# Performance work log

Measured on AMD Instinct MI355X. Metric: run time of the kernel, lower is better.

## Reference

```python
import jax, jax.numpy as jnp
import numpy as np

B, L, D = 1, 2048, 2048
H, KVH, HD = 16, 4, 128
E, TOPK, G, TKG = 16, 4, 4, 2   # experts, top_k, n_group, topk_group
I, SH_I = 1024, 2048            # moe_intermediate, shared intermediate (1024*2)
EPS = 1e-5
THETA = 1e6
SCALE = HD ** -0.5
RSF = 2.5                        # routed_scaling_factor


def rms(x, w):
    return x * jax.lax.rsqrt(jnp.mean(x * x, axis=-1, keepdims=True) + EPS) * w


def rope(x):
    # x: [B, n_heads, L, HD], non-traditional (split-half) RoPE
    pos = jnp.arange(x.shape[2], dtype=jnp.float32)
    inv = 1.0 / (THETA ** (jnp.arange(0, HD, 2, dtype=jnp.float32) / HD))
    ang = pos[:, None] * inv[None, :]                    # [L, HD/2]
    cos, sin = jnp.cos(ang), jnp.sin(ang)
    x1, x2 = x[..., : HD // 2], x[..., HD // 2 :]
    return jnp.concatenate([x1 * cos - x2 * sin, x2 * cos + x1 * sin], axis=-1)


def setup_inputs() -> dict:
    key = jax.random.key(0)
    ks = jax.random.split(key, 13)
    s = 0.02
    mk = lambda k, shp: jax.random.normal(k, shp, jnp.float32) * s
    return {
        'x': jax.random.normal(ks[0], (B, L, D), jnp.float32),
        'w_q': mk(ks[1], (H * HD, D)),
        'w_k': mk(ks[2], (KVH * HD, D)),
        'w_v': mk(ks[3], (KVH * HD, D)),
        'w_o': mk(ks[4], (D, H * HD)),
        'q_norm_w': jnp.ones(HD, jnp.float32),
        'k_norm_w': jnp.ones(HD, jnp.float32),
        'ln1_w': jnp.ones(D, jnp.float32),
        'ln2_w': jnp.ones(D, jnp.float32),
        'gate_w': mk(ks[5], (E, D)),
        'gate_bias': mk(ks[6], (E,)),
        'wg': mk(ks[7], (E, I, D)),
        'wu': mk(ks[8], (E, I, D)),
        'wd': mk(ks[9], (E, D, I)),
        'sh_g': mk(ks[10], (SH_I, D)),
        'sh_u': mk(ks[11], (SH_I, D)),
        'sh_d': mk(ks[12], (D, SH_I)),
    }


def reference(x, w_q, w_k, w_v, w_o, q_norm_w, k_norm_w, ln1_w, ln2_w,
              gate_w, gate_bias, wg, wu, wd, sh_g, sh_u, sh_d):
    # ---- attention block ----
    h = rms(x, ln1_w)
    q = rms((h @ w_q.T).reshape(B, L, H, HD), q_norm_w).transpose(0, 2, 1, 3)
    k = rms((h @ w_k.T).reshape(B, L, KVH, HD), k_norm_w).transpose(0, 2, 1, 3)
    v = (h @ w_v.T).reshape(B, L, KVH, HD).transpose(0, 2, 1, 3)
    q, k = rope(q), rope(k)
    rep = H // KVH
    k = jnp.repeat(k, rep, axis=1)
    v = jnp.repeat(v, rep, axis=1)
    causal = jnp.tril(jnp.ones((L, L), bool))
    logits = jnp.einsum('bhqd,bhkd->bhqk', q, k) * SCALE
    logits = jnp.where(causal, logits, jnp.float32(-1e30))
    attn = jax.nn.softmax(logits, axis=-1)
    o = jnp.einsum('bhqk,bhkd->bhqd', attn, v).transpose(0, 2, 1, 3).reshape(B, L, H * HD)
    h1 = x + o @ w_o.T

    # ---- MoE block ----
    t = rms(h1, ln2_w).reshape(B * L, D)
    T = t.shape[0]
    # group-limited top-k gate (noaux_tc)
    sc = jax.nn.sigmoid(t @ gate_w.T)                    # [T, E] original scores
    s2 = sc + gate_bias
    sg = s2.reshape(T, G, E // G)
    group_scores = jax.lax.top_k(sg, 2)[0].sum(-1)       # [T, G]
    gidx = jax.lax.top_k(group_scores, TKG)[1]           # keep TKG best groups
    gmask = jnp.zeros((T, G), jnp.float32).at[jnp.arange(T)[:, None], gidx].set(1.0)
    masked = (sg * gmask[..., None]).reshape(T, E)       # dropped groups -> 0
    inds = jax.lax.top_k(masked, TOPK)[1]                # [T, TOPK]
    w = jnp.take_along_axis(sc, inds, axis=-1)
    w = w / (w.sum(-1, keepdims=True) + 1e-20) * RSF
    # combine weights scattered into [T, E]
    C = jnp.zeros((T, E), jnp.float32).at[jnp.arange(T)[:, None], inds].add(w)
    # expert SwiGLU (dense over experts, masked combine -> identical math)
    g = jnp.einsum('td,eid->tei', t, wg)
    u = jnp.einsum('td,eid->tei', t, wu)
    hm = jax.nn.silu(g) * u                               # [T, E, I]
    y = jnp.einsum('tei,edi,te->td', hm, wd, C)
    # shared experts
    sh = (jax.nn.silu(t @ sh_g.T) * (t @ sh_u.T)) @ sh_d.T
    return h1 + (y + sh).reshape(B, L, D)
```

## Files before the change

### kernel.cpp

```cpp
#include <hip/hip_runtime.h>
#include <math.h>

#define TT 2048
#define DM 2048
#define NHD 16
#define NKV 4
#define HDIM 128
#define NI 1024
#define ATT_SCALE 0.08838834764831845f

typedef unsigned short u16;
typedef __attribute__((ext_vector_type(8))) short short8;
typedef __attribute__((ext_vector_type(4))) short short4v;
typedef __attribute__((ext_vector_type(4))) float float4v;

#define AS1 __attribute__((address_space(1)))
#define AS3 __attribute__((address_space(3)))

__device__ __forceinline__ u16 f2bf(float f) {
  union { float f; unsigned u; } v; v.f = f;
  unsigned r = v.u + 0x7fffu + ((v.u >> 16) & 1u);
  return (u16)(r >> 16);
}
__device__ __forceinline__ float bf2f(u16 h) {
  union { unsigned u; float f; } v; v.u = ((unsigned)h) << 16;
  return v.f;
}
__device__ __forceinline__ float4v mfma16(short8 a, short8 b, float4v c) {
  return __builtin_amdgcn_mfma_f32_16x16x32_bf16(a, b, c, 0, 0, 0);
}
__device__ __forceinline__ void gl_lds(const u16* g, u16* l) {
  __builtin_amdgcn_global_load_lds((const AS1 void*)g, (AS3 void*)l, 16, 0, 0);
}

__global__ void cvt_split(const float* __restrict__ s, u16* __restrict__ oh,
                          u16* __restrict__ ol, int n) {
  int i = (blockIdx.x * 256 + threadIdx.x) * 4;
  if (i >= n) return;
  float4v v = *(const float4v*)(s + i);
  short4v vh, vl;
  #pragma unroll
  for (int c = 0; c < 4; ++c) {
    u16 hb = f2bf(v[c]);
    vh[c] = (short)hb;
    vl[c] = (short)f2bf(v[c] - bf2f(hb));
  }
  *(short4v*)(oh + i) = vh;
  *(short4v*)(ol + i) = vl;
}

__global__ void cvt_plain(const float* __restrict__ s, u16* __restrict__ o, int n) {
  int i = (blockIdx.x * 256 + threadIdx.x) * 8;
  if (i >= n) return;
  float4v v0 = *(const float4v*)(s + i);
  float4v v1 = *(const float4v*)(s + i + 4);
  short8 ov;
  #pragma unroll
  for (int c = 0; c < 4; ++c) {
    ov[c] = (short)f2bf(v0[c]);
    ov[c + 4] = (short)f2bf(v1[c]);
  }
  *(short8*)(o + i) = ov;
}

__global__ void rms_kernel(const float* __restrict__ in, const float* __restrict__ w,
                           u16* oh, u16* ol, float* of, u16* ob) {
  const int row = blockIdx.x, tid = threadIdx.x;
  const int lane = tid & 63, wvi = tid >> 6;
  const float* xr = in + (long)row * DM;
  float4v a = *(const float4v*)(xr + tid * 4);
  float4v b = *(const float4v*)(xr + 1024 + tid * 4);
  float ss = a[0]*a[0] + a[1]*a[1] + a[2]*a[2] + a[3]*a[3]
           + b[0]*b[0] + b[1]*b[1] + b[2]*b[2] + b[3]*b[3];
  #pragma unroll
  for (int m = 1; m < 64; m <<= 1) ss += __shfl_xor(ss, m);
  __shared__ float red[4];
  if (lane == 0) red[wvi] = ss;
  __syncthreads();
  float tot = red[0] + red[1] + red[2] + red[3];
  float sc = 1.0f / sqrtf(tot * (1.0f / 2048.0f) + 1e-5f);
  float4v w0 = *(const float4v*)(w + tid * 4);
  float4v w1 = *(const float4v*)(w + 1024 + tid * 4);
  #pragma unroll
  for (int c = 0; c < 4; ++c) {
    float v0 = a[c] * sc * w0[c];
    float v1 = b[c] * sc * w1[c];
    long i0 = (long)row * DM + tid * 4 + c;
    long i1 = i0 + 1024;
    if (oh) {
      u16 h0 = f2bf(v0); oh[i0] = h0; ol[i0] = f2bf(v0 - bf2f(h0));
      u16 h1 = f2bf(v1); oh[i1] = h1; ol[i1] = f2bf(v1 - bf2f(h1));
    }
    if (of) { of[i0] = v0; of[i1] = v1; }
    if (ob) { ob[i0] = f2bf(v0); ob[i1] = f2bf(v1); }
  }
}

__global__ void rope_kernel(const float* __restrict__ qlin, const float* __restrict__ klin,
                            const float* __restrict__ qw, const float* __restrict__ kw,
                            u16* qh, u16* ql, u16* kh, u16* kl) {
  int rw = blockIdx.x * 4 + (threadIdx.x >> 6);
  int lane = threadIdx.x & 63;
  int t = rw / 20, hh = rw - t * 20;
  const float* src; const float* nw; u16 *dh, *dl;
  if (hh < 16) {
    long ofs = (long)t * 2048 + hh * 128;
    src = qlin + ofs; nw = qw; dh = qh + ofs; dl = ql + ofs;
  } else {
    long ofs = (long)t * 512 + (hh - 16) * 128;
    src = klin + ofs; nw = kw; dh = kh + ofs; dl = kl + ofs;
  }
  float x1 = src[lane], x2 = src[lane + 64];
  float ss = x1 * x1 + x2 * x2;
  #pragma unroll
  for (int m = 1; m < 64; m <<= 1) ss += __shfl_xor(ss, m);
  float sc = 1.0f / sqrtf(ss * (1.0f / 128.0f) + 1e-5f);
  x1 *= sc * nw[lane];
  x2 *= sc * nw[lane + 64];
  double inv = pow(1.0e6, -(double)lane * (1.0 / 64.0));
  double ang = (double)t * inv;
  float cs = (float)cos(ang), sn = (float)sin(ang);
  float o1 = x1 * cs - x2 * sn;
  float o2 = x2 * cs + x1 * sn;
  u16 hb1 = f2bf(o1); dh[lane] = hb1;      dl[lane] = f2bf(o1 - bf2f(hb1));
  u16 hb2 = f2bf(o2); dh[lane + 64] = hb2; dl[lane + 64] = f2bf(o2 - bf2f(hb2));
}

struct GemmP {
  const u16* Ah; long aloOff;
  const u16* B0h; const u16* B1h; long blo0; long blo1; long bstride; int ns0;
  int K;
  const int* permA; const int* cnt; const int* offs;
  int fixedM; int maxRow;
  float* oF; int ldF;
  float* oF2; int ldF2; int osplit;
  u16* oB; long oBlo; int ldB;
  const float* addX;
  const u16* dslots; const int* inv;
};

template<int EPI, bool SPLIT>
__launch_bounds__(256, 2)
__global__ void gemm_bt(GemmP p) {
  const int e = blockIdx.z;
  const int cnt = p.cnt ? p.cnt[e] : p.fixedM;
  const int mt0 = blockIdx.x * 128;
  if (mt0 >= cnt) return;
  const int off = p.offs ? p.offs[e] : 0;
  const int nt0 = blockIdx.y * 128;

  __shared__ u16 lAh[128 * 64];
  __shared__ u16 lBh[128 * 64];
  __shared__ u16 lAl[SPLIT ? 128 * 64 : 8];
  __shared__ u16 lBl[SPLIT ? 128 * 64 : 8];

  const int tid = threadIdx.x;
  const int lane = tid & 63, wvi = tid >> 6;
  const int quad = lane >> 4, l16 = lane & 15;
  const int wm = (wvi >> 1) * 64, wn = (wvi & 1) * 64;
  const int srow = tid >> 3;
  const int scc = (tid & 7) ^ (srow & 7);

  const u16* agp[4];
  #pragma unroll
  for (int i = 0; i < 4; ++i) {
    int m = mt0 + i * 32 + srow;
    int r = off + m; if (r > p.maxRow) r = p.maxRow;
    if (p.permA) r = p.permA[r];
    agp[i] = p.Ah + (long)r * p.K + scc * 8;
  }
  const u16* bgph[4]; const u16* bgpl[4];
  #pragma unroll
  for (int j = 0; j < 4; ++j) {
    int n = nt0 + j * 32 + srow;
    const u16* bp; long lo;
    if (n < p.ns0) { bp = p.B0h + (long)e * p.bstride + (long)n * p.K; lo = p.blo0; }
    else           { bp = p.B1h + (long)e * p.bstride + (long)(n - p.ns0) * p.K; lo = p.blo1; }
    bgph[j] = bp + scc * 8;
    bgpl[j] = bp + lo + scc * 8;
  }

  float4v acc[4][4];
  #pragma unroll
  for (int a = 0; a < 4; ++a)
    #pragma unroll
    for (int b = 0; b < 4; ++b)
      acc[a][b] = (float4v){0.f, 0.f, 0.f, 0.f};

  const int wofs = wvi * 64 * 8;

  for (int k0 = 0; k0 < p.K; k0 += 64) {
    __syncthreads();
    #pragma unroll
    for (int i = 0; i < 4; ++i) {
      gl_lds(agp[i] + k0, &lAh[i * 2048 + wofs]);
      if constexpr (SPLIT) gl_lds(agp[i] + p.aloOff + k0, &lAl[i * 2048 + wofs]);
    }
    #pragma unroll
    for (int j = 0; j < 4; ++j) {
      gl_lds(bgph[j] + k0, &lBh[j * 2048 + wofs]);
      if constexpr (SPLIT) gl_lds(bgpl[j] + k0, &lBl[j * 2048 + wofs]);
    }
    __syncthreads();
    #pragma unroll
    for (int kc = 0; kc < 2; ++kc) {
      short8 ah[4], al[4], bh[4], bl[4];
      #pragma unroll
      for (int t = 0; t < 4; ++t) {
        int m = wm + t * 16 + l16;
        int ia = (m * 8 + ((kc * 4 + quad) ^ (m & 7))) * 8;
        ah[t] = *(const short8*)&lAh[ia];
        if constexpr (SPLIT) al[t] = *(const short8*)&lAl[ia];
        int n = wn + t * 16 + l16;
        int ib = (n * 8 + ((kc * 4 + quad) ^ (n & 7))) * 8;
        bh[t] = *(const short8*)&lBh[ib];
        if constexpr (SPLIT) bl[t] = *(const short8*)&lBl[ib];
      }
      #pragma unroll
      for (int mt = 0; mt < 4; ++mt)
        #pragma unroll
        for (int nt = 0; nt < 4; ++nt) {
          acc[mt][nt] = mfma16(ah[mt], bh[nt], acc[mt][nt]);
          if constexpr (SPLIT) {
            acc[mt][nt] = mfma16(ah[mt], bl[nt], acc[mt][nt]);
            acc[mt][nt] = mfma16(al[mt], bh[nt], acc[mt][nt]);
          }
        }
    }
  }

  #pragma unroll
  for (int mt = 0; mt < 4; ++mt) {
    #pragma unroll
    for (int nt = 0; nt < 4; ++nt) {
      const int n = nt0 + wn + nt * 16 + l16;
      const int mlb = wm + mt * 16 + quad * 4;
      if constexpr (EPI == 1) {
        short4v vh, vl;
        #pragma unroll
        for (int r = 0; r < 4; ++r) {
          float v = acc[mt][nt][r];
          u16 hb = f2bf(v);
          vh[r] = (short)hb;
          vl[r] = (short)f2bf(v - bf2f(hb));
        }
        long ix = (long)n * p.ldB + (mt0 + mlb);
        *(short4v*)&p.oB[ix] = vh;
        *(short4v*)&p.oB[ix + p.oBlo] = vl;
      } else {
        #pragma unroll
        for (int r = 0; r < 4; ++r) {
          const int gm = mt0 + mlb + r;
          if (gm >= cnt) continue;
          float v = acc[mt][nt][r];
          if constexpr (EPI == 0) {
            if (n < p.osplit) p.oF[(long)gm * p.ldF + n] = v;
            else p.oF2[(long)gm * p.ldF2 + (n - p.osplit)] = v;
          } else if constexpr (EPI == 2) {
            long ix = (long)gm * p.ldF + n;
            p.oF[ix] = v + p.addX[ix];
          } else if constexpr (EPI == 3) {
            p.oB[(long)(off + gm) * p.ldB + n] = f2bf(v);
          } else if constexpr (EPI == 5) {
            long ix = (long)gm * p.ldF + n;
            const int* iv = p.inv + gm * 4;
            float s = bf2f(p.dslots[(long)iv[0] * DM + n])
                    + bf2f(p.dslots[(long)iv[1] * DM + n])
                    + bf2f(p.dslots[(long)iv[2] * DM + n])
                    + bf2f(p.dslots[(long)iv[3] * DM + n]);
            p.oF[ix] = v + p.addX[ix] + s;
          }
        }
      }
    }
  }
}

__launch_bounds__(256, 2)
__global__ void attn_kernel(const u16* __restrict__ qh, const u16* __restrict__ ql,
                            const u16* __restrict__ kh, const u16* __restrict__ kl,
                            const u16* __restrict__ vh, const u16* __restrict__ vl,
                            u16* __restrict__ oh, u16* __restrict__ ol) {
  const int head = blockIdx.x;
  const int qt = 31 - (int)blockIdx.y;
  const int kvh = head >> 2;
  const int tid = threadIdx.x;
  const int lane = tid & 63, wvi = tid >> 6;
  const int quad = lane >> 4, l16 = lane & 15;

  __shared__ u16 lKh[64 * 128];
  __shared__ u16 lKl[64 * 128];
  __shared__ u16 lVh[128 * 64];
  __shared__ u16 lVl[128 * 64];
  __shared__ u16 lP[4][2][16 * 64];
  u16* Ph = &lP[wvi][0][0];
  u16* Pl = &lP[wvi][1][0];

  const int qbase = qt * 64;
  const int qrow0 = qbase + wvi * 16;
  short8 qfh[4], qfl[4];
  {
    int row = qrow0 + l16;
    const u16* ph = qh + (long)row * (NHD * HDIM) + head * HDIM + quad * 8;
    const u16* pl = ql + (long)row * (NHD * HDIM) + head * HDIM + quad * 8;
    #pragma unroll
    for (int kc = 0; kc < 4; ++kc) {
      qfh[kc] = *(const short8*)(ph + kc * 32);
      qfl[kc] = *(const short8*)(pl + kc * 32);
    }
  }
  float4v oacc[8];
  #pragma unroll
  for (int dt = 0; dt < 8; ++dt) oacc[dt] = (float4v){0.f, 0.f, 0.f, 0.f};
  float mrun[4], lrun[4];
  #pragma unroll
  for (int r = 0; r < 4; ++r) { mrun[r] = -INFINITY; lrun[r] = 0.f; }

  const int sck = (tid & 15) ^ (tid >> 4);
  const int scv = (tid & 7) ^ ((tid >> 3) & 7);
  const int nsteps = qt + 1;

  for (int kt = 0; kt < nsteps; ++kt) {
    const int t0 = kt * 64;
    __syncthreads();
    #pragma unroll
    for (int i = 0; i < 4; ++i) {
      int krow = i * 16 + (tid >> 4);
      long kg = (long)(t0 + krow) * (NKV * HDIM) + kvh * HDIM + sck * 8;
      gl_lds(kh + kg, &lKh[(i * 256 + wvi * 64) * 8]);
      gl_lds(kl + kg, &lKl[(i * 256 + wvi * 64) * 8]);
      int vrow = i * 32 + (tid >> 3);
      long vg = (long)(kvh * HDIM + vrow) * TT + t0 + scv * 8;
      gl_lds(vh + vg, &lVh[(i * 256 + wvi * 64) * 8]);
      gl_lds(vl + vg, &lVl[(i * 256 + wvi * 64) * 8]);
    }
    __syncthreads();

    float4v s[4];
    #pragma unroll
    for (int nt = 0; nt < 4; ++nt) s[nt] = (float4v){0.f, 0.f, 0.f, 0.f};
    #pragma unroll
    for (int kc = 0; kc < 4; ++kc) {
      #pragma unroll
      for (int nt = 0; nt < 4; ++nt) {
        int n = nt * 16 + l16;
        int idx = (n * 16 + ((kc * 4 + quad) ^ (n & 15))) * 8;
        short8 bh = *(const short8*)&lKh[idx];
        short8 bl = *(const short8*)&lKl[idx];
        s[nt] = mfma16(qfh[kc], bh, s[nt]);
        s[nt] = mfma16(qfh[kc], bl, s[nt]);
        s[nt] = mfma16(qfl[kc], bh, s[nt]);
      }
    }

    const bool dg = (kt == qt);
    #pragma unroll
    for (int nt = 0; nt < 4; ++nt)
      #pragma unroll
      for (int r = 0; r < 4; ++r) {
        float v = s[nt][r] * ATT_SCALE;
        if (dg) {
          int kcol = t0 + nt * 16 + l16;
          int qrow = qrow0 + quad * 4 + r;
          if (kcol > qrow) v = -1e30f;
        }
        s[nt][r] = v;
      }

    float alf[4];
    #pragma unroll
    for (int r = 0; r < 4; ++r) {
      float mx = fmaxf(fmaxf(s[0][r], s[1][r]), fmaxf(s[2][r], s[3][r]));
      mx = fmaxf(mx, __shfl_xor(mx, 1));
      mx = fmaxf(mx, __shfl_xor(mx, 2));
      mx = fmaxf(mx, __shfl_xor(mx, 4));
      mx = fmaxf(mx, __shfl_xor(mx, 8));
      float mnew = fmaxf(mrun[r], mx);
      float al = expf(mrun[r] - mnew);
      float ps = 0.f;
      #pragma unroll
      for (int nt = 0; nt < 4; ++nt) {
        float pv = expf(s[nt][r] - mnew);
        s[nt][r] = pv;
        ps += pv;
      }
      ps += __shfl_xor(ps, 1); ps += __shfl_xor(ps, 2);
      ps += __shfl_xor(ps, 4); ps += __shfl_xor(ps, 8);
      lrun[r] = lrun[r] * al + ps;
      mrun[r] = mnew;
      alf[r] = al;
    }
    #pragma unroll
    for (int dt = 0; dt < 8; ++dt)
      #pragma unroll
      for (int r = 0; r < 4; ++r)
        oacc[dt][r] *= alf[r];

    #pragma unroll
    for (int nt = 0; nt < 4; ++nt)
      #pragma unroll
      for (int r = 0; r < 4; ++r) {
        int row = quad * 4 + r;
        int col = nt * 16 + l16;
        int idx = (row * 8 + ((col >> 3) ^ (row & 7))) * 8 + (col & 7);
        float pv = s[nt][r];
        u16 hb = f2bf(pv);
        Ph[idx] = hb;
        Pl[idx] = f2bf(pv - bf2f(hb));
      }

    #pragma unroll
    for (int kc = 0; kc < 2; ++kc) {
      int idxp = (l16 * 8 + ((kc * 4 + quad) ^ (l16 & 7))) * 8;
      short8 ph = *(const short8*)&Ph[idxp];
      short8 pl = *(const short8*)&Pl[idxp];
      #pragma unroll
      for (int dt = 0; dt < 8; ++dt) {
        int d = dt * 16 + l16;
        int idx = (d * 8 + ((kc * 4 + quad) ^ (d & 7))) * 8;
        short8 wh = *(const short8*)&lVh[idx];
        short8 wl = *(const short8*)&lVl[idx];
        oacc[dt] = mfma16(ph, wh, oacc[dt]);
        oacc[dt] = mfma16(ph, wl, oacc[dt]);
        oacc[dt] = mfma16(pl, wh, oacc[dt]);
      }
    }
  }

  #pragma unroll
  for (int dt = 0; dt < 8; ++dt)
    #pragma unroll
    for (int r = 0; r < 4; ++r) {
      int row = qrow0 + quad * 4 + r;
      int d = dt * 16 + l16;
      float v = oacc[dt][r] / lrun[r];
      long ix = (long)row * (NHD * HDIM) + head * HDIM + d;
      u16 hb = f2bf(v);
      oh[ix] = hb;
      ol[ix] = f2bf(v - bf2f(hb));
    }
}

__global__ void routing_kernel(const float* __restrict__ t32, const float* __restrict__ gw,
                               const float* __restrict__ gb,
                               int* inds, float* wv, int* counts) {
  int t = blockIdx.x;
  int lane = threadIdx.x;
  const float* tr = t32 + (long)t * DM;
  float4v tv[8];
  #pragma unroll
  for (int j = 0; j < 8; ++j) tv[j] = *(const float4v*)(tr + lane * 32 + j * 4);
  float sc[16];
  for (int e = 0; e < 16; ++e) {
    const float* g = gw + (long)e * DM + lane * 32;
    float acc = 0.f;
    #pragma unroll
    for (int j = 0; j < 8; ++j) {
      float4v gv = *(const float4v*)(g + j * 4);
      acc += tv[j][0]*gv[0] + tv[j][1]*gv[1] + tv[j][2]*gv[2] + tv[j][3]*gv[3];
    }
    #pragma unroll
    for (int m = 1; m < 64; m <<= 1) acc += __shfl_xor(acc, m);
    sc[e] = 1.f / (1.f + expf(-acc));
  }
  if (lane == 0) {
    float s2[16];
    for (int e = 0; e < 16; ++e) s2[e] = sc[e] + gb[e];
    float gs[4];
    for (int g = 0; g < 4; ++g) {
      float xq[4] = { s2[4*g], s2[4*g+1], s2[4*g+2], s2[4*g+3] };
      int am = 0; float m1 = xq[0];
      for (int i = 1; i < 4; ++i) if (xq[i] > m1) { m1 = xq[i]; am = i; }
      float m2 = -1e30f;
      for (int i = 0; i < 4; ++i) if (i != am) m2 = fmaxf(m2, xq[i]);
      gs[g] = m1 + m2;
    }
    int g0 = 0;
    for (int g = 1; g < 4; ++g) if (gs[g] > gs[g0]) g0 = g;
    int g1 = -1;
    for (int g = 0; g < 4; ++g) if (g != g0 && (g1 < 0 || gs[g] > gs[g1])) g1 = g;
    float msk[16];
    for (int e = 0; e < 16; ++e) {
      int g = e >> 2;
      msk[e] = (g == g0 || g == g1) ? s2[e] : 0.0f;
    }
    int id[4]; float w[4]; float wsum = 0.f;
    for (int j = 0; j < 4; ++j) {
      int bi = 0; float bv = msk[0];
      for (int e = 1; e < 16; ++e) if (msk[e] > bv) { bv = msk[e]; bi = e; }
      id[j] = bi; w[j] = sc[bi]; msk[bi] = -1e30f;
      wsum += w[j];
    }
    float scale = 2.5f / (wsum + 1e-20f);
    for (int j = 0; j < 4; ++j) {
      inds[t * 4 + j] = id[j];
      wv[t * 4 + j] = w[j] * scale;
      atomicAdd(&counts[id[j]], 1);
    }
  }
}

__global__ void scan_kernel(int* ctrl) {
  if (threadIdx.x == 0) {
    int a = 0;
    for (int e = 0; e < 16; ++e) { ctrl[16 + e] = a; a += ctrl[e]; }
  }
}

__global__ void assign_kernel(const int* inds, const float* wv, int* ctrl,
                              int* perm, float* wslot, int* inv) {
  int t = blockIdx.x * 256 + threadIdx.x;
  if (t >= TT) return;
  for (int j = 0; j < 4; ++j) {
    int e = inds[t * 4 + j];
    int pos = atomicAdd(&ctrl[32 + e], 1);
    int s = ctrl[16 + e] + pos;
    perm[s] = t;
    wslot[s] = wv[t * 4 + j];
    inv[t * 4 + j] = s;
  }
}

__global__ void hm_moe_kernel(const u16* __restrict__ gu, const float* __restrict__ wslot,
                              u16* __restrict__ hm) {
  int slot = blockIdx.x;
  int i = threadIdx.x * 4;
  float w = wslot[slot];
  const u16* gp = gu + (long)slot * 2048;
  short4v gv = *(const short4v*)(gp + i);
  short4v uv = *(const short4v*)(gp + 1024 + i);
  short4v ov;
  #pragma unroll
  for (int c = 0; c < 4; ++c) {
    float g = bf2f((u16)gv[c]);
    float u = bf2f((u16)uv[c]);
    float h = g / (1.f + expf(-g)) * u * w;
    ov[c] = (short)f2bf(h);
  }
  *(short4v*)&hm[(long)slot * 1024 + i] = ov;
}

__global__ void hm_sh_kernel(const u16* __restrict__ gu, u16* __restrict__ hm) {
  int t = blockIdx.x;
  int i = threadIdx.x * 8;
  const u16* gp = gu + (long)t * 4096 + i;
  const u16* up = gu + (long)t * 4096 + 2048 + i;
  u16* op = hm + (long)t * 2048 + i;
  #pragma unroll
  for (int c = 0; c < 2; ++c) {
    short4v gv = *(const short4v*)(gp + c * 4);
    short4v uv = *(const short4v*)(up + c * 4);
    short4v ov;
    #pragma unroll
    for (int q = 0; q < 4; ++q) {
      float g = bf2f((u16)gv[q]);
      float u = bf2f((u16)uv[q]);
      float h = g / (1.f + expf(-g)) * u;
      ov[q] = (short)f2bf(h);
    }
    *(short4v*)(op + c * 4) = ov;
  }
}

extern "C" void kernel_launch(void* const* d_in, const int* in_sizes, int n_in,
                              void* d_out, int out_size, void* d_ws, size_t ws_size,
                              hipStream_t stream) {
  (void)in_sizes; (void)n_in; (void)out_size; (void)ws_size;
  const float* x   = (const float*)d_in[0];
  const float* wq  = (const float*)d_in[1];
  const float* wk  = (const float*)d_in[2];
  const float* wvv = (const float*)d_in[3];
  const float* wo  = (const float*)d_in[4];
  const float* qnw = (const float*)d_in[5];
  const float* knw = (const float*)d_in[6];
  const float* ln1 = (const float*)d_in[7];
  const float* ln2 = (const float*)d_in[8];
  const float* gw  = (const float*)d_in[9];
  const float* gb  = (const float*)d_in[10];
  const float* wg  = (const float*)d_in[11];
  const float* wu  = (const float*)d_in[12];
  const float* wd  = (const float*)d_in[13];
  const float* shg = (const float*)d_in[14];
  const float* shu = (const float*)d_in[15];
  const float* shd = (const float*)d_in[16];
  float* out = (float*)d_out;

  char* wp = (char*)d_ws;
  auto alloc = [&](size_t b) -> char* { char* r = wp; wp += (b + 255) & ~(size_t)255; return r; };
  u16* h_hi   = (u16*)alloc((size_t)TT * DM * 2);
  u16* h_lo   = (u16*)alloc((size_t)TT * DM * 2);
  float* q_lin = (float*)alloc((size_t)TT * 2048 * 4);
  float* k_lin = (float*)alloc((size_t)TT * 512 * 4);
  u16* q_hi   = (u16*)alloc((size_t)TT * 2048 * 2);
  u16* q_lo   = (u16*)alloc((size_t)TT * 2048 * 2);
  u16* k_hi   = (u16*)alloc((size_t)TT * 512 * 2);
  u16* k_lo   = (u16*)alloc((size_t)TT * 512 * 2);
  u16* vT_hi  = (u16*)alloc((size_t)512 * TT * 2);
  u16* vT_lo  = (u16*)alloc((size_t)512 * TT * 2);
  u16* o_hi   = (u16*)alloc((size_t)TT * 2048 * 2);
  u16* o_lo   = (u16*)alloc((size_t)TT * 2048 * 2);
  float* h1   = (float*)alloc((size_t)TT * DM * 4);
  float* t32  = (float*)alloc((size_t)TT * DM * 4);
  u16* t_bf   = (u16*)alloc((size_t)TT * DM * 2);
  u16* gu_sh  = (u16*)alloc((size_t)TT * 4096 * 2);
  u16* hm_sh  = (u16*)alloc((size_t)TT * 2048 * 2);
  u16* gu_moe = (u16*)alloc((size_t)8192 * 2048 * 2);
  u16* hm_moe = (u16*)alloc((size_t)8192 * 1024 * 2);
  u16* dtmp   = (u16*)alloc((size_t)8192 * 2048 * 2);
  int* inds   = (int*)alloc((size_t)TT * 4 * 4);
  float* wvals = (float*)alloc((size_t)TT * 4 * 4);
  int* ctrl   = (int*)alloc(256);
  int* perm   = (int*)alloc(8192 * 4);
  float* wslot = (float*)alloc(8192 * 4);
  int* inv    = (int*)alloc((size_t)TT * 4 * 4);
  const int NQ = 2048 * 2048, NK = 512 * 2048;
  u16* wq_c  = (u16*)alloc((size_t)NQ * 2 * 2);
  u16* wk_c  = (u16*)alloc((size_t)NK * 2 * 2);
  u16* wv_c  = (u16*)alloc((size_t)NK * 2 * 2);
  u16* wo_c  = (u16*)alloc((size_t)NQ * 2 * 2);
  const int NGU = 16 * NI * DM;
  u16* wg_c  = (u16*)alloc((size_t)NGU * 2);
  u16* wu_c  = (u16*)alloc((size_t)NGU * 2);
  u16* wd_c  = (u16*)alloc((size_t)NGU * 2);
  u16* shg_c = (u16*)alloc((size_t)NQ * 2);
  u16* shu_c = (u16*)alloc((size_t)NQ * 2);
  u16* shd_c = (u16*)alloc((size_t)NQ * 2);

  hipMemsetAsync(ctrl, 0, 256, stream);

  cvt_split<<<NQ / 4 / 256, 256, 0, stream>>>(wq, wq_c, wq_c + NQ, NQ);
  cvt_split<<<NK / 4 / 256, 256, 0, stream>>>(wk, wk_c, wk_c + NK, NK);
  cvt_split<<<NK / 4 / 256, 256, 0, stream>>>(wvv, wv_c, wv_c + NK, NK);
  cvt_split<<<NQ / 4 / 256, 256, 0, stream>>>(wo, wo_c, wo_c + NQ, NQ);
  cvt_plain<<<NGU / 8 / 256, 256, 0, stream>>>(wg, wg_c, NGU);
  cvt_plain<<<NGU / 8 / 256, 256, 0, stream>>>(wu, wu_c, NGU);
  cvt_plain<<<NGU / 8 / 256, 256, 0, stream>>>(wd, wd_c, NGU);
  cvt_plain<<<NQ / 8 / 256, 256, 0, stream>>>(shg, shg_c, NQ);
  cvt_plain<<<NQ / 8 / 256, 256, 0, stream>>>(shu, shu_c, NQ);
  cvt_plain<<<NQ / 8 / 256, 256, 0, stream>>>(shd, shd_c, NQ);

  rms_kernel<<<TT, 256, 0, stream>>>(x, ln1, h_hi, h_lo, nullptr, nullptr);

  { GemmP p{}; p.Ah = h_hi; p.aloOff = h_lo - h_hi;
    p.B0h = wq_c; p.blo0 = NQ; p.B1h = wk_c; p.blo1 = NK; p.ns0 = 2048;
    p.K = DM; p.fixedM = TT; p.maxRow = TT - 1;
    p.oF = q_lin; p.ldF = 2048; p.oF2 = k_lin; p.ldF2 = 512; p.osplit = 2048;
    gemm_bt<0, true><<<dim3(16, 20, 1), 256, 0, stream>>>(p); }

  { GemmP p{}; p.Ah = h_hi; p.aloOff = h_lo - h_hi;
    p.B0h = wv_c; p.blo0 = NK; p.B1h = wv_c; p.blo1 = NK; p.ns0 = 1 << 30;
    p.K = DM; p.fixedM = TT; p.maxRow = TT - 1;
    p.oB = vT_hi; p.oBlo = vT_lo - vT_hi; p.ldB = TT;
    gemm_bt<1, true><<<dim3(16, 4, 1), 256, 0, stream>>>(p); }

  rope_kernel<<<TT * 20 / 4, 256, 0, stream>>>(q_lin, k_lin, qnw, knw, q_hi, q_lo, k_hi, k_lo);

  attn_kernel<<<dim3(NHD, 32, 1), 256, 0, stream>>>(q_hi, q_lo, k_hi, k_lo, vT_hi, vT_lo, o_hi, o_lo);

  { GemmP p{}; p.Ah = o_hi; p.aloOff = o_lo - o_hi;
    p.B0h = wo_c; p.blo0 = NQ; p.B1h = wo_c; p.blo1 = NQ; p.ns0 = 1 << 30;
    p.K = DM; p.fixedM = TT; p.maxRow = TT - 1;
    p.oF = h1; p.ldF = 2048; p.addX = x;
    gemm_bt<2, true><<<dim3(16, 16, 1), 256, 0, stream>>>(p); }

  rms_kernel<<<TT, 256, 0, stream>>>(h1, ln2, nullptr, nullptr, t32, t_bf);

  routing_kernel<<<TT, 64, 0, stream>>>(t32, gw, gb, inds, wvals, ctrl);
  scan_kernel<<<1, 64, 0, stream>>>(ctrl);
  assign_kernel<<<8, 256, 0, stream>>>(inds, wvals, ctrl, perm, wslot, inv);

  { GemmP p{}; p.Ah = t_bf; p.B0h = shg_c; p.B1h = shu_c; p.ns0 = 2048; p.K = DM;
    p.fixedM = TT; p.maxRow = TT - 1; p.oB = gu_sh; p.ldB = 4096;
    gemm_bt<3, false><<<dim3(16, 32, 1), 256, 0, stream>>>(p); }
  hm_sh_kernel<<<TT, 256, 0, stream>>>(gu_sh, hm_sh);

  { GemmP p{}; p.Ah = t_bf; p.permA = perm; p.cnt = ctrl; p.offs = ctrl + 16;
    p.fixedM = TT; p.maxRow = 8191;
    p.B0h = wg_c; p.B1h = wu_c; p.ns0 = 1024; p.bstride = (long)NI * DM; p.K = DM;
    p.oB = gu_moe; p.ldB = 2048;
    gemm_bt<3, false><<<dim3(16, 16, 16), 256, 0, stream>>>(p); }
  hm_moe_kernel<<<8192, 256, 0, stream>>>(gu_moe, wslot, hm_moe);
  { GemmP p{}; p.Ah = hm_moe; p.cnt = ctrl; p.offs = ctrl + 16;
    p.fixedM = TT; p.maxRow = 8191;
    p.B0h = wd_c; p.B1h = wd_c; p.ns0 = 1 << 30; p.bstride = (long)DM * NI; p.K = NI;
    p.oB = dtmp; p.ldB = 2048;
    gemm_bt<3, false><<<dim3(16, 16, 16), 256, 0, stream>>>(p); }

  { GemmP p{}; p.Ah = hm_sh; p.B0h = shd_c; p.B1h = shd_c; p.ns0 = 1 << 30; p.K = DM;
    p.fixedM = TT; p.maxRow = TT - 1;
    p.oF = out; p.ldF = 2048; p.addX = h1; p.dslots = dtmp; p.inv = inv;
    gemm_bt<5, false><<<dim3(16, 16, 1), 256, 0, stream>>>(p); }
}
```

Baseline: 1.549 ms.

## Prefetch next GEMM K-tile into registers to overlap loads with MFMA

Replaces the direct global-to-LDS loads in the GEMM main loop with register prefetching. The next K-tile is loaded into registers while MFMAs run on the current tile, then stored to LDS at the top of the next iteration, so global latency is hidden behind compute. Launch bounds for the non-split variant are raised to allow 4 blocks per CU. The prefetch buffers add register pressure, which could force spills or lower occupancy, especially in the split (hi/lo) variant.

After: 2.793 ms. 80.3% more time.

```diff
diff --git a/kernel.cpp b/kernel.cpp
--- a/kernel.cpp
+++ b/kernel.cpp
@@ -140,7 +140,7 @@
 };
 
 template<int EPI, bool SPLIT>
-__launch_bounds__(256, 2)
+__launch_bounds__(256, SPLIT ? 2 : 4)
 __global__ void gemm_bt(GemmP p) {
   const int e = blockIdx.z;
   const int cnt = p.cnt ? p.cnt[e] : p.fixedM;
@@ -188,20 +188,42 @@
       acc[a][b] = (float4v){0.f, 0.f, 0.f, 0.f};
 
   const int wofs = wvi * 64 * 8;
+  const int ldso = wofs + lane * 8;
+
+  short8 rAh[4], rAl[4], rBh[4], rBl[4];
+  #pragma unroll
+  for (int i = 0; i < 4; ++i) {
+    rAh[i] = *(const short8*)(agp[i]);
+    rBh[i] = *(const short8*)(bgph[i]);
+    if constexpr (SPLIT) {
+      rAl[i] = *(const short8*)(agp[i] + p.aloOff);
+      rBl[i] = *(const short8*)(bgpl[i]);
+    }
+  }
 
   for (int k0 = 0; k0 < p.K; k0 += 64) {
     __syncthreads();
     #pragma unroll
     for (int i = 0; i < 4; ++i) {
-      gl_lds(agp[i] + k0, &lAh[i * 2048 + wofs]);
-      if constexpr (SPLIT) gl_lds(agp[i] + p.aloOff + k0, &lAl[i * 2048 + wofs]);
-    }
-    #pragma unroll
-    for (int j = 0; j < 4; ++j) {
-      gl_lds(bgph[j] + k0, &lBh[j * 2048 + wofs]);
-      if constexpr (SPLIT) gl_lds(bgpl[j] + k0, &lBl[j * 2048 + wofs]);
+      *(short8*)&lAh[i * 2048 + ldso] = rAh[i];
+      *(short8*)&lBh[i * 2048 + ldso] = rBh[i];
+      if constexpr (SPLIT) {
+        *(short8*)&lAl[i * 2048 + ldso] = rAl[i];
+        *(short8*)&lBl[i * 2048 + ldso] = rBl[i];
+      }
     }
     __syncthreads();
+    if (k0 + 64 < p.K) {
+      #pragma unroll
+      for (int i = 0; i < 4; ++i) {
+        rAh[i] = *(const short8*)(agp[i] + k0 + 64);
+        rBh[i] = *(const short8*)(bgph[i] + k0 + 64);
+        if constexpr (SPLIT) {
+          rAl[i] = *(const short8*)(agp[i] + p.aloOff + k0 + 64);
+          rBl[i] = *(const short8*)(bgpl[i] + k0 + 64);
+        }
+      }
+    }
     #pragma unroll
     for (int kc = 0; kc < 2; ++kc) {
       short8 ah[4], al[4], bh[4], bl[4];
```
